# Kernel optimization log

Hardware: AMD Instinct MI355X
Metric: run time of the kernel (lower is better)

Reference implementation:

```python
import jax, jax.numpy as jnp
import numpy as np

B, H, E, IN, OUT = 4096, 1, 8, 256, 256

# BinActive: forward sign(x), backward straight-through clipped to |x|<=1
@jax.custom_vjp
def bin_active(x):
    return jnp.sign(x)

def _ba_fwd(x):
    return jnp.sign(x), x

def _ba_bwd(x, g):
    return (g * (jnp.abs(x) <= 1.0).astype(g.dtype),)

bin_active.defvjp(_ba_fwd, _ba_bwd)

# BinarySoftActivation_Head: hard-threshold gate at 0.5, identity STE backward
@jax.custom_vjp
def bin_gate(x):
    return (x > 0.5).astype(x.dtype)

def _bg_fwd(x):
    return (x > 0.5).astype(x.dtype), None

def _bg_bwd(_, g):
    return (g,)

bin_gate.defvjp(_bg_fwd, _bg_bwd)


def setup_inputs() -> dict:
    key = jax.random.key(0)
    k1, k2, k3, k4, k5 = jax.random.split(key, 5)
    x = jax.random.normal(k1, (B, H, IN), dtype=jnp.float32)
    weight = jax.random.normal(k2, (H, E, IN, OUT), dtype=jnp.float32) * 0.05
    proj_w = jax.random.normal(k3, (E, IN), dtype=jnp.float32) * 0.05  # nn.Linear weight [out,in]
    proj_b = jax.random.normal(k4, (E,), dtype=jnp.float32) * 0.05
    scale = jax.random.normal(k5, (H, 1, OUT), dtype=jnp.float32) * 0.1
    return {"x": x, "weight": weight, "proj_w": proj_w, "proj_b": proj_b, "scale": scale}


def reference(x, weight, proj_w, proj_b, scale):
    # x: [B, H, in]; weight: [H, E, in, out]; proj_w: [E, in]; proj_b: [E]; scale: [H, 1, out]
    xh = jnp.transpose(x, (1, 0, 2))                              # [H, B, in]
    gate = jax.nn.sigmoid(jnp.einsum('hbi,ei->hbe', xh, proj_w) + proj_b)
    gate = bin_gate(gate)                                         # hard 0/1 gates [H, B, E]
    # per-sample synthesized weight (the huge intermediate): [H, B, in, out]
    w = jnp.einsum('hbe,heio->hbio', gate, weight)
    xb = bin_active(xh)                                           # sign-binarized activations
    wb = bin_active(w)                                            # sign-binarized weights
    y = jnp.einsum('hbi,hbio->hbo', xb, wb)                       # batched GEMV, [H, B, out]
    y = y * scale                                                 # per-head learned scale
    return jnp.transpose(y, (1, 0, 2))                            # [B, H, out]
```

## Files before the change

kernel.cpp:

```cpp
#include <hip/hip_runtime.h>
#include <stdint.h>

#define B_N   4096
#define E_N   8
#define IN_N  256
#define OUT_N 256
#define NMASK 256

__global__ __launch_bounds__(256) void build_wbits(const float* __restrict__ W,
                                                   uint64_t* __restrict__ wbits) {
    const int lane = threadIdx.x & 63;
    const int wv   = threadIdx.x >> 6;
    const int o    = blockIdx.x * 4 + wv;
    const int j    = blockIdx.y;
    const int i    = j * 64 + lane;

    float w[E_N];
    #pragma unroll
    for (int e = 0; e < E_N; ++e)
        w[e] = W[((size_t)e * IN_N + i) * OUT_N + o];

    float slo[16];
    slo[0] = 0.0f;
    #pragma unroll
    for (int m = 1; m < 16; ++m) {
        const int hb = 31 - __builtin_clz(m);
        slo[m] = slo[m ^ (1 << hb)] + w[hb];
    }

    #pragma unroll 1
    for (int lo = 0; lo < 16; ++lo) {
        float t[16];
        t[0] = slo[lo];
        #pragma unroll
        for (int h = 1; h < 16; ++h) {
            const int hb = 31 - __builtin_clz(h);
            t[h] = t[h ^ (1 << hb)] + w[4 + hb];
        }
        #pragma unroll
        for (int h = 0; h < 16; ++h) {
            const int mask = h * 16 + lo;
            const unsigned long long bits = __ballot(t[h] < 0.0f);
            if (lane == 0)
                wbits[((size_t)mask * OUT_N + o) * 4 + j] = bits;
        }
    }
}

__global__ __launch_bounds__(256) void gate_gemv(const float* __restrict__ x,
                                                 const float* __restrict__ pw,
                                                 const float* __restrict__ pb,
                                                 const float* __restrict__ scale,
                                                 const uint64_t* __restrict__ wbits,
                                                 float* __restrict__ out) {
    const int b    = blockIdx.x;
    const int t    = threadIdx.x;
    const int wave = t >> 6;
    const int lane = t & 63;

    __shared__ float              partial[4][E_N];
    __shared__ unsigned long long xw[4], zw[4];
    __shared__ uint32_t           mask_s;

    const float xi = x[(size_t)b * IN_N + t];

    const unsigned long long sb = __ballot(xi < 0.0f);
    const unsigned long long zb = __ballot(xi == 0.0f);
    if (lane == 0) { xw[wave] = sb; zw[wave] = zb; }

    #pragma unroll
    for (int e = 0; e < E_N; ++e) {
        float v = xi * pw[e * IN_N + t];
        v += __shfl_down(v, 32); v += __shfl_down(v, 16); v += __shfl_down(v, 8);
        v += __shfl_down(v, 4);  v += __shfl_down(v, 2);  v += __shfl_down(v, 1);
        if (lane == 0) partial[wave][e] = v;
    }
    __syncthreads();

    if (t == 0) {
        uint32_t m = 0;
        #pragma unroll
        for (int e = 0; e < E_N; ++e) {
            const float z = ((partial[0][e] + partial[1][e]) +
                             (partial[2][e] + partial[3][e])) + pb[e];
            if (z > 0.0f) m |= (1u << e);
        }
        mask_s = m;
    }
    __syncthreads();

    const uint32_t m = mask_s;
    float y = 0.0f;
    if (m != 0u) {
        const uint64_t* wp = wbits + ((size_t)m * OUT_N + t) * 4;
        const ulonglong2 wa = *reinterpret_cast<const ulonglong2*>(wp);
        const ulonglong2 wb2 = *reinterpret_cast<const ulonglong2*>(wp + 2);
        const uint64_t x0 = xw[0], x1 = xw[1], x2 = xw[2], x3 = xw[3];
        const uint64_t z0 = zw[0], z1 = zw[1], z2 = zw[2], z3 = zw[3];
        const int nz = __popcll(z0) + __popcll(z1) + __popcll(z2) + __popcll(z3);
        const int d  = __popcll((x0 ^ wa.x) & ~z0)
                     + __popcll((x1 ^ wa.y) & ~z1)
                     + __popcll((x2 ^ wb2.x) & ~z2)
                     + __popcll((x3 ^ wb2.y) & ~z3);
        y = (float)(IN_N - nz - 2 * d) * scale[t];
    }
    out[(size_t)b * OUT_N + t] = y;
}

extern "C" void kernel_launch(void* const* d_in, const int* in_sizes, int n_in,
                              void* d_out, int out_size, void* d_ws, size_t ws_size,
                              hipStream_t stream) {
    const float* x     = (const float*)d_in[0];
    const float* W     = (const float*)d_in[1];
    const float* pw    = (const float*)d_in[2];
    const float* pb    = (const float*)d_in[3];
    const float* scale = (const float*)d_in[4];
    float*       out   = (float*)d_out;

    uint64_t* wbits = (uint64_t*)d_ws;

    hipLaunchKernelGGL(build_wbits, dim3(OUT_N / 4, 4), dim3(256), 0, stream,
                       W, wbits);
    hipLaunchKernelGGL(gate_gemv, dim3(B_N), dim3(256), 0, stream,
                       x, pw, pb, scale, wbits, out);
}
```

Measured before the change: 93.66 us.

## Process one sample per wave in gate_gemv, removing shared memory and barriers

Each wavefront now handles a whole batch row: it loads four x values per lane, builds sign and zero bitmasks by ballot, and computes the gate logits with a full-wave xor-shuffle reduction. This removes the shared-memory partials and both block barriers. Each lane then produces four outputs from the packed weight bits. The grid shrinks by four, which trades per-block sync overhead for more work per thread.

```diff
diff --git a/kernel.cpp b/kernel.cpp
--- a/kernel.cpp
+++ b/kernel.cpp
@@ -53,58 +53,57 @@
                                                  const float* __restrict__ scale,
                                                  const uint64_t* __restrict__ wbits,
                                                  float* __restrict__ out) {
-    const int b    = blockIdx.x;
-    const int t    = threadIdx.x;
-    const int wave = t >> 6;
-    const int lane = t & 63;
+    const int lane = threadIdx.x & 63;
+    const int wv   = threadIdx.x >> 6;
+    const int b    = blockIdx.x * 4 + wv;
 
-    __shared__ float              partial[4][E_N];
-    __shared__ unsigned long long xw[4], zw[4];
-    __shared__ uint32_t           mask_s;
+    const float* xb = x + (size_t)b * IN_N;
+    float xs[4];
+    #pragma unroll
+    for (int j = 0; j < 4; ++j) xs[j] = xb[j * 64 + lane];
 
-    const float xi = x[(size_t)b * IN_N + t];
+    uint64_t xw[4], zw[4];
+    #pragma unroll
+    for (int j = 0; j < 4; ++j) {
+        xw[j] = __ballot(xs[j] <  0.0f);
+        zw[j] = __ballot(xs[j] == 0.0f);
+    }
 
-    const unsigned long long sb = __ballot(xi < 0.0f);
-    const unsigned long long zb = __ballot(xi == 0.0f);
-    if (lane == 0) { xw[wave] = sb; zw[wave] = zb; }
-
+    uint32_t mask = 0u;
     #pragma unroll
     for (int e = 0; e < E_N; ++e) {
-        float v = xi * pw[e * IN_N + t];
-        v += __shfl_down(v, 32); v += __shfl_down(v, 16); v += __shfl_down(v, 8);
-        v += __shfl_down(v, 4);  v += __shfl_down(v, 2);  v += __shfl_down(v, 1);
-        if (lane == 0) partial[wave][e] = v;
+        const float* pwe = pw + e * IN_N;
+        float v = xs[0] * pwe[lane];
+        v += xs[1] * pwe[ 64 + lane];
+        v += xs[2] * pwe[128 + lane];
+        v += xs[3] * pwe[192 + lane];
+        v += __shfl_xor(v, 1);  v += __shfl_xor(v, 2);  v += __shfl_xor(v, 4);
+        v += __shfl_xor(v, 8);  v += __shfl_xor(v, 16); v += __shfl_xor(v, 32);
+        if (v + pb[e] > 0.0f) mask |= (1u << e);
     }
-    __syncthreads();
 
-    if (t == 0) {
-        uint32_t m = 0;
+    float* ob = out + (size_t)b * OUT_N;
+    if (mask != 0u) {
+        const uint64_t* wp = wbits + (size_t)mask * (OUT_N * 4);
+        const int nz = __popcll(zw[0]) + __popcll(zw[1]) +
+                       __popcll(zw[2]) + __popcll(zw[3]);
+        const int base = IN_N - nz;
         #pragma unroll
-        for (int e = 0; e < E_N; ++e) {
-            const float z = ((partial[0][e] + partial[1][e]) +
-                             (partial[2][e] + partial[3][e])) + pb[e];
-            if (z > 0.0f) m |= (1u << e);
+        for (int q = 0; q < 4; ++q) {
+            const int o = q * 64 + lane;
+            const uint64_t* w4 = wp + (size_t)o * 4;
+            const ulonglong2 a  = *reinterpret_cast<const ulonglong2*>(w4);
+            const ulonglong2 c  = *reinterpret_cast<const ulonglong2*>(w4 + 2);
+            const int d = __popcll((xw[0] ^ a.x) & ~zw[0])
+                        + __popcll((xw[1] ^ a.y) & ~zw[1])
+                        + __popcll((xw[2] ^ c.x) & ~zw[2])
+                        + __popcll((xw[3] ^ c.y) & ~zw[3]);
+            ob[o] = (float)(base - 2 * d) * scale[o];
         }
-        mask_s = m;
+    } else {
+        #pragma unroll
+        for (int q = 0; q < 4; ++q) ob[q * 64 + lane] = 0.0f;
     }
-    __syncthreads();
-
-    const uint32_t m = mask_s;
-    float y = 0.0f;
-    if (m != 0u) {
-        const uint64_t* wp = wbits + ((size_t)m * OUT_N + t) * 4;
-        const ulonglong2 wa = *reinterpret_cast<const ulonglong2*>(wp);
-        const ulonglong2 wb2 = *reinterpret_cast<const ulonglong2*>(wp + 2);
-        const uint64_t x0 = xw[0], x1 = xw[1], x2 = xw[2], x3 = xw[3];
-        const uint64_t z0 = zw[0], z1 = zw[1], z2 = zw[2], z3 = zw[3];
-        const int nz = __popcll(z0) + __popcll(z1) + __popcll(z2) + __popcll(z3);
-        const int d  = __popcll((x0 ^ wa.x) & ~z0)
-                     + __popcll((x1 ^ wa.y) & ~z1)
-                     + __popcll((x2 ^ wb2.x) & ~z2)
-                     + __popcll((x3 ^ wb2.y) & ~z3);
-        y = (float)(IN_N - nz - 2 * d) * scale[t];
-    }
-    out[(size_t)b * OUT_N + t] = y;
 }
 
 extern "C" void kernel_launch(void* const* d_in, const int* in_sizes, int n_in,
@@ -121,6 +120,6 @@
 
     hipLaunchKernelGGL(build_wbits, dim3(OUT_N / 4, 4), dim3(256), 0, stream,
                        W, wbits);
-    hipLaunchKernelGGL(gate_gemv, dim3(B_N), dim3(256), 0, stream,
+    hipLaunchKernelGGL(gate_gemv, dim3(B_N / 4), dim3(256), 0, stream,
                        x, pw, pb, scale, wbits, out);
 }
```

Result: faster. 82.23 us (-12.2%).
